# Performance work log

Hardware: AMD Instinct MI355X
Metric: run time of the kernel (lower is better)

## Reference

```python
import jax, jax.numpy as jnp
import numpy as np

HIDDEN = 4096
N_HEADS = 32
N_KV_HEADS = 8
HEAD_DIM = 128
ROPE_THETA = 10000.0


def setup_inputs() -> dict:
    key = jax.random.key(0)
    ks = jax.random.split(key, 5)
    B, S = 1, 2048
    scale = 0.02
    return {
        "hidden_states": jax.random.normal(ks[0], (B, S, HIDDEN), dtype=jnp.float32),
        "q_w": jax.random.normal(ks[1], (N_HEADS * HEAD_DIM, HIDDEN), dtype=jnp.float32) * scale,
        "k_w": jax.random.normal(ks[2], (N_KV_HEADS * HEAD_DIM, HIDDEN), dtype=jnp.float32) * scale,
        "v_w": jax.random.normal(ks[3], (N_KV_HEADS * HEAD_DIM, HIDDEN), dtype=jnp.float32) * scale,
        "o_w": jax.random.normal(ks[4], (HIDDEN, N_HEADS * HEAD_DIM), dtype=jnp.float32) * scale,
        "position_ids": jnp.arange(S, dtype=jnp.int64 if jax.config.jax_enable_x64 else jnp.int32)[None, :],
    }


def _rotate_half(x):
    h = x.shape[-1] // 2
    return jnp.concatenate((-x[..., h:], x[..., :h]), axis=-1)


def _rope_cos_sin(position_ids, dtype):
    # default rope: inv_freq = theta^(-arange(0,hd,2)/hd), attention_scaling = 1
    inv_freq = 1.0 / (ROPE_THETA ** (jnp.arange(0, HEAD_DIM, 2, dtype=jnp.float32) / HEAD_DIM))
    freqs = position_ids.astype(jnp.float32)[:, :, None] * inv_freq[None, None, :]  # [B,S,hd/2]
    emb = jnp.concatenate((freqs, freqs), axis=-1)  # [B,S,hd]
    return jnp.cos(emb).astype(dtype), jnp.sin(emb).astype(dtype)


def reference(hidden_states, q_w, k_w, v_w, o_w, position_ids):
    B, S, _ = hidden_states.shape
    n_rep = N_HEADS // N_KV_HEADS

    q = (hidden_states @ q_w.T).reshape(B, S, N_HEADS, HEAD_DIM).transpose(0, 2, 1, 3)
    k = (hidden_states @ k_w.T).reshape(B, S, N_KV_HEADS, HEAD_DIM).transpose(0, 2, 1, 3)
    v = (hidden_states @ v_w.T).reshape(B, S, N_KV_HEADS, HEAD_DIM).transpose(0, 2, 1, 3)

    cos, sin = _rope_cos_sin(position_ids, hidden_states.dtype)
    cos = cos[:, None, :, :]  # unsqueeze head dim
    sin = sin[:, None, :, :]
    q = q * cos + _rotate_half(q) * sin
    k = k * cos + _rotate_half(k) * sin

    # repeat_kv (GQA)
    k = jnp.repeat(k, n_rep, axis=1)  # [B,H,S,hd]
    v = jnp.repeat(v, n_rep, axis=1)

    scale = HEAD_DIM ** -0.5
    scores = jnp.einsum("bhqd,bhkd->bhqk", q, k) * scale  # [B,H,S,S]
    causal = jnp.tril(jnp.ones((S, S), dtype=bool))
    scores = jnp.where(causal[None, None, :, :], scores, jnp.finfo(scores.dtype).min)
    probs = jax.nn.softmax(scores, axis=-1)
    attn = jnp.einsum("bhqk,bhkd->bhqd", probs, v)  # [B,H,S,hd]

    attn = attn.transpose(0, 2, 1, 3).reshape(B, S, N_HEADS * HEAD_DIM)
    return attn @ o_w.T
```

## Files before the change

kernel.cpp:

```cpp
#include <hip/hip_runtime.h>
#include <hip/hip_bf16.h>

#define NH   32
#define NKV  8
#define HD   128
#define SL   2048
#define HID  4096
#define KVW  1024
#define QKVN 6144

typedef __attribute__((ext_vector_type(8))) short short8;
typedef __attribute__((ext_vector_type(4))) float f32x4;

static __device__ __forceinline__ unsigned short f2bf(float f){
  union { float f; unsigned int i; } v; v.f = f;
  unsigned int r = v.i + 0x7FFFu + ((v.i >> 16) & 1u);
  return (unsigned short)(r >> 16);
}
static __device__ __forceinline__ float bf2f(unsigned short u){
  union { unsigned int i; float f; } v; v.i = ((unsigned int)u) << 16; return v.f;
}
static __device__ __forceinline__ unsigned int pack2(float lo, float hi){
  return (unsigned int)f2bf(lo) | ((unsigned int)f2bf(hi) << 16);
}
static __device__ __forceinline__ unsigned int cvtpk(float lo, float hi){
  unsigned int d;
  asm("v_cvt_pk_bf16_f32 %0, %1, %2" : "=v"(d) : "v"(lo), "v"(hi));
  return d;
}

static __device__ __forceinline__ void gload_lds16(const void* g, void* l){
  __builtin_amdgcn_global_load_lds(
      (const __attribute__((address_space(1))) void*)g,
      (__attribute__((address_space(3))) void*)l,
      16, 0, 0);
}

__global__ void cast_f32_bf16(const float* __restrict__ src, uint4* __restrict__ dst, int n8){
  int stride = gridDim.x * blockDim.x;
  for (int i = blockIdx.x * blockDim.x + threadIdx.x; i < n8; i += stride){
    float4 a = ((const float4*)src)[2*i + 0];
    float4 b = ((const float4*)src)[2*i + 1];
    uint4 o;
    o.x = pack2(a.x, a.y); o.y = pack2(a.z, a.w);
    o.z = pack2(b.x, b.y); o.w = pack2(b.z, b.w);
    dst[i] = o;
  }
}

__global__ void rope_table_kernel(const int* __restrict__ pos, float2* __restrict__ tab){
  int i = blockIdx.x * blockDim.x + threadIdx.x;
  if (i >= SL * 64) return;
  int s = i >> 6, f = i & 63;
  float inv = expf(-((float)(2 * f) / 128.0f) * 9.210340371976184f);
  float ang = (float)pos[s] * inv;
  float sn, cs;
  sincosf(ang, &sn, &cs);
  tab[i] = make_float2(cs, sn);
}

__global__ void rope_apply_kernel(unsigned short* x, const float2* __restrict__ tab,
                                  int nheads, int rowstride){
  int i = blockIdx.x * blockDim.x + threadIdx.x;
  int total = SL * nheads * 8;
  if (i >= total) return;
  int fb = (i & 7) * 8;
  int t = i >> 3;
  int h = t % nheads;
  int s = t / nheads;
  size_t base = (size_t)s * rowstride + h * HD;
  short8 x1 = *(const short8*)&x[base + fb];
  short8 x2 = *(const short8*)&x[base + fb + 64];
  const float2* tb = &tab[s * 64 + fb];
  short8 o1, o2;
#pragma unroll
  for (int j = 0; j < 8; ++j){
    float2 cs = tb[j];
    float a = bf2f((unsigned short)x1[j]);
    float b = bf2f((unsigned short)x2[j]);
    o1[j] = (short)f2bf(a * cs.x - b * cs.y);
    o2[j] = (short)f2bf(b * cs.x + a * cs.y);
  }
  *(short8*)&x[base + fb]      = o1;
  *(short8*)&x[base + fb + 64] = o2;
}

template<int BN, bool F32OUT>
__global__ __launch_bounds__(256) void gemm_bt(
  const unsigned short* __restrict__ A,
  const unsigned short* __restrict__ B,
  void* __restrict__ Cp, int M, int N, int K)
{
  constexpr int NFR = BN / 32;
  __shared__ __align__(16) unsigned short As[2][128 * 32];
  __shared__ __align__(16) unsigned short Bs[2][BN * 32];
  const int tid = threadIdx.x;
  const int lane = tid & 63, wid = tid >> 6;
  const int g = lane >> 4, c15 = lane & 15;
  const int wr = wid >> 1, wc = wid & 1;

  const int gx = gridDim.x, gy = gridDim.y;
  const int nwg = gx * gy;
  const int lin = blockIdx.y * gx + blockIdx.x;
  int mb, nb;
  const int cpx = nwg >> 3;
  const int RN  = cpx >> 3;
  if (RN > 0 && (gy & 7) == 0 && (cpx & 7) == 0 && gx % RN == 0 && (8 % (gx / RN)) == 0){
    int xcd = lin & 7, j = lin >> 3;
    int nrc = gx / RN;
    int rr = xcd / nrc, rc = xcd % nrc;
    mb = rr * 8 + (j & 7);
    nb = rc * RN + (j >> 3);
  } else { mb = lin / gx; nb = lin % gx; }
  const int m0 = mb * 128, n0 = nb * BN;

  const int srowA = wid * 32 + (lane >> 2);
  const int srowB = wid * (BN / 4) + (lane >> 2);
  const int scol  = (lane & 3) * 8;
  const unsigned short* Ag = &A[(size_t)(m0 + srowA) * K + scol];
  const unsigned short* Bg = &B[(size_t)(n0 + srowB) * K + scol];
  const size_t K16 = (size_t)16 * K;

  f32x4 acc[4][NFR] = {};

  gload_lds16(Ag,       &As[0][wid * 1024]);
  gload_lds16(Ag + K16, &As[0][wid * 1024 + 512]);
#pragma unroll
  for (int q = 0; q < BN / 64; ++q)
    gload_lds16(Bg + q * K16, &Bs[0][wid * (BN / 4) * 32 + q * 512]);
  __syncthreads();

  const int nk = K >> 5;
  for (int t = 0; t < nk; ++t){
    const int cur = t & 1;
    if (t + 1 < nk){
      const unsigned short* a2 = Ag + (size_t)(t + 1) * 32;
      const unsigned short* b2 = Bg + (size_t)(t + 1) * 32;
      const int nb2 = cur ^ 1;
      gload_lds16(a2,       &As[nb2][wid * 1024]);
      gload_lds16(a2 + K16, &As[nb2][wid * 1024 + 512]);
#pragma unroll
      for (int q = 0; q < BN / 64; ++q)
        gload_lds16(b2 + q * K16, &Bs[nb2][wid * (BN / 4) * 32 + q * 512]);
    }
    short8 af[4], bfr[NFR];
#pragma unroll
    for (int m = 0; m < 4; ++m)
      af[m] = *(const short8*)(&As[cur][(wr * 64 + m * 16 + c15) * 32 + g * 8]);
#pragma unroll
    for (int n = 0; n < NFR; ++n)
      bfr[n] = *(const short8*)(&Bs[cur][(wc * (BN / 2) + n * 16 + c15) * 32 + g * 8]);
#pragma unroll
    for (int m = 0; m < 4; ++m)
#pragma unroll
      for (int n = 0; n < NFR; ++n)
        acc[m][n] = __builtin_amdgcn_mfma_f32_16x16x32_bf16(af[m], bfr[n], acc[m][n], 0, 0, 0);
    __syncthreads();
  }

#pragma unroll
  for (int m = 0; m < 4; ++m)
#pragma unroll
    for (int n = 0; n < NFR; ++n){
      int row = m0 + wr * 64 + m * 16 + g * 4;
      int col = n0 + wc * (BN / 2) + n * 16 + c15;
      f32x4 v = acc[m][n];
      if (F32OUT){
        float* C = (float*)Cp;
#pragma unroll
        for (int r = 0; r < 4; ++r) C[(size_t)(row + r) * N + col] = v[r];
      } else {
        unsigned short* C = (unsigned short*)Cp;
#pragma unroll
        for (int r = 0; r < 4; ++r) C[(size_t)(row + r) * N + col] = f2bf(v[r]);
      }
    }
}

__global__ void transpose_v_kernel(const unsigned short* __restrict__ v, int vstride,
                                   unsigned short* __restrict__ vt){
  __shared__ unsigned short t[64][65];
  int h  = blockIdx.z;
  int d0 = blockIdx.y * 64;
  int s0 = blockIdx.x * 64;
  int c  = threadIdx.x & 63;
  int r0 = threadIdx.x >> 6;
#pragma unroll
  for (int r = r0; r < 64; r += 4) t[r][c] = v[(size_t)(s0 + r) * vstride + h * HD + d0 + c];
  __syncthreads();
#pragma unroll
  for (int r = r0; r < 64; r += 4) vt[(size_t)(h * HD + d0 + r) * SL + s0 + c] = t[c][r];
}

__global__ __launch_bounds__(512, 4) void flash_attn_kernel(
  const unsigned short* __restrict__ Q,
  const unsigned short* __restrict__ Kb,
  const unsigned short* __restrict__ Vt,
  unsigned short* __restrict__ O)
{
  __shared__ __align__(16) unsigned short Ks[2][64 * 128];
  __shared__ __align__(16) unsigned short Vs[2][128 * 64];
  const int tid = threadIdx.x, lane = tid & 63, wid = tid >> 6;
  const int g = lane >> 4, c15 = lane & 15;
  const int kvh = blockIdx.x;
  const int yy = blockIdx.y;
  const int qb = (yy < 32) ? (63 - yy) : (yy - 32);
  const int h = kvh * 4 + (wid & 3);
  const int rg = wid >> 2;
  const int q0 = qb * 32;
  const int qg = q0 + rg * 16 + c15;

  short8 aq[4];
  {
    size_t qrow = (size_t)qg * QKVN + h * HD;
#pragma unroll
    for (int kk = 0; kk < 4; ++kk)
      aq[kk] = *(const short8*)(&Q[qrow + kk * 32 + g * 8]);
  }

  const int krow = tid >> 3, kcol = (tid & 7) * 8;
  const int vrow = tid >> 2, vcol = (tid & 3) * 8;
  const unsigned short* Kgb = Kb + (size_t)kvh * HD;
  const unsigned short* Vgb = Vt + ((size_t)kvh * HD + vrow) * SL;

  auto loadKV = [&](int kt, uint4& a, uint4& b, uint4& c, uint4& d){
    const unsigned short* kg = Kgb + (size_t)(kt * 64 + krow) * QKVN + kcol;
    a = *(const uint4*)kg; b = *(const uint4*)(kg + 64);
    const unsigned short* vg = Vgb + kt * 64 + vcol;
    c = *(const uint4*)vg; d = *(const uint4*)(vg + 32);
  };
  auto writeKV = [&](int buf, uint4 a, uint4 b, uint4 c, uint4 d){
    *(uint4*)((char*)&Ks[buf][0] + krow * 256 + (( kcol * 2       ) ^ ((krow & 7) << 4))) = a;
    *(uint4*)((char*)&Ks[buf][0] + krow * 256 + (((kcol * 2) + 128) ^ ((krow & 7) << 4))) = b;
    *(uint4*)((char*)&Vs[buf][0] + vrow * 128 + (( vcol * 2       ) ^ ((vrow & 7) << 4))) = c;
    *(uint4*)((char*)&Vs[buf][0] + vrow * 128 + (((vcol * 2) +  64) ^ ((vrow & 7) << 4))) = d;
  };

  float m_i = -1e30f, l_i = 0.f;
  f32x4 oacc[8];
#pragma unroll
  for (int df = 0; df < 8; ++df) oacc[df] = (f32x4){0.f, 0.f, 0.f, 0.f};

  const float scl2 = 0.08838834764831845f * 1.4426950408889634f;
  const int nt = (q0 + 31) / 64 + 1;

  uint4 kr0, kr1, vr0, vr1;
  loadKV(0, kr0, kr1, vr0, vr1);
  writeKV(0, kr0, kr1, vr0, vr1);
  if (nt > 1) loadKV(1, kr0, kr1, vr0, vr1);
  __syncthreads();

  for (int kt = 0; kt < nt; ++kt){
    const int cur = kt & 1, nxt = cur ^ 1;
    if (kt + 1 < nt) writeKV(nxt, kr0, kr1, vr0, vr1);
    if (kt + 2 < nt) loadKV(kt + 2, kr0, kr1, vr0, vr1);

    f32x4 sc[4];
    __builtin_amdgcn_s_setprio(1);
#pragma unroll
    for (int f = 0; f < 4; ++f){
      sc[f] = (f32x4){0.f, 0.f, 0.f, 0.f};
#pragma unroll
      for (int kk = 0; kk < 4; ++kk){
        short8 bk = *(const short8*)((const char*)&Ks[cur][0] + (f * 16 + c15) * 256 +
                                     ((kk * 64 + g * 16) ^ ((c15 & 7) << 4)));
        sc[f] = __builtin_amdgcn_mfma_f32_16x16x32_bf16(bk, aq[kk], sc[f], 0, 0, 0);
      }
    }
    __builtin_amdgcn_s_setprio(0);

    float p[4][4];
    if (kt * 64 + 63 <= q0 + rg * 16){
#pragma unroll
      for (int f = 0; f < 4; ++f)
#pragma unroll
        for (int r = 0; r < 4; ++r) p[f][r] = sc[f][r] * scl2;
    } else {
#pragma unroll
      for (int f = 0; f < 4; ++f)
#pragma unroll
        for (int r = 0; r < 4; ++r){
          int kvg = kt * 64 + f * 16 + g * 4 + r;
          p[f][r] = (kvg <= qg) ? sc[f][r] * scl2 : -1e30f;
        }
    }

    float pmax = p[0][0];
#pragma unroll
    for (int f = 0; f < 4; ++f)
#pragma unroll
      for (int r = 0; r < 4; ++r) pmax = fmaxf(pmax, p[f][r]);
    pmax = fmaxf(pmax, __shfl_xor(pmax, 16, 64));
    pmax = fmaxf(pmax, __shfl_xor(pmax, 32, 64));

    if (!__all(pmax - m_i <= 8.0f)){
      float mnew = fmaxf(m_i, pmax);
      float cf = exp2f(m_i - mnew);
      float cfr[4];
#pragma unroll
      for (int r = 0; r < 4; ++r) cfr[r] = __shfl(cf, (lane & 48) | (g * 4 + r), 64);
#pragma unroll
      for (int df = 0; df < 8; ++df)
#pragma unroll
        for (int r = 0; r < 4; ++r) oacc[df][r] *= cfr[r];
      l_i *= cf;
      m_i = mnew;
    }

    float lsum = 0.f;
#pragma unroll
    for (int f = 0; f < 4; ++f)
#pragma unroll
      for (int r = 0; r < 4; ++r){ float e = exp2f(p[f][r] - m_i); p[f][r] = e; lsum += e; }
    lsum += __shfl_xor(lsum, 16, 64);
    lsum += __shfl_xor(lsum, 32, 64);
    l_i += lsum;

    unsigned int pd[4][2];
#pragma unroll
    for (int f = 0; f < 4; ++f){
      pd[f][0] = cvtpk(p[f][0], p[f][1]);
      pd[f][1] = cvtpk(p[f][2], p[f][3]);
    }

    const int src0 = ((g & 1) << 5) | c15;
    const int src1 = src0 + 16;
    const bool hiF = (g >= 2);
#pragma unroll
    for (int kk = 0; kk < 2; ++kk){
      union { unsigned int u[4]; short8 s8; } pa;
#pragma unroll
      for (int pr = 0; pr < 2; ++pr){
        unsigned int a0 = __shfl((int)pd[2 * kk + 0][pr], src0, 64);
        unsigned int b0 = __shfl((int)pd[2 * kk + 1][pr], src0, 64);
        unsigned int a1 = __shfl((int)pd[2 * kk + 0][pr], src1, 64);
        unsigned int b1 = __shfl((int)pd[2 * kk + 1][pr], src1, 64);
        pa.u[pr]     = hiF ? b0 : a0;
        pa.u[2 + pr] = hiF ? b1 : a1;
      }
      __builtin_amdgcn_s_setprio(1);
#pragma unroll
      for (int df = 0; df < 8; ++df){
        short8 bv = *(const short8*)((const char*)&Vs[cur][0] + (df * 16 + c15) * 128 +
                                     ((kk * 64 + g * 16) ^ ((c15 & 7) << 4)));
        oacc[df] = __builtin_amdgcn_mfma_f32_16x16x32_bf16(pa.s8, bv, oacc[df], 0, 0, 0);
      }
      __builtin_amdgcn_s_setprio(0);
    }
    __syncthreads();
  }

  float lr[4];
#pragma unroll
  for (int r = 0; r < 4; ++r) lr[r] = __shfl(l_i, (lane & 48) | (g * 4 + r), 64);
#pragma unroll
  for (int df = 0; df < 8; ++df)
#pragma unroll
    for (int r = 0; r < 4; ++r){
      int row = q0 + rg * 16 + g * 4 + r;
      O[(size_t)row * HID + h * HD + df * 16 + c15] = f2bf(oacc[df][r] / lr[r]);
    }
}

extern "C" void kernel_launch(void* const* d_in, const int* in_sizes, int n_in,
                              void* d_out, int out_size, void* d_ws, size_t ws_size,
                              hipStream_t stream)
{
  const float* hs  = (const float*)d_in[0];
  const float* qw  = (const float*)d_in[1];
  const float* kw  = (const float*)d_in[2];
  const float* vw  = (const float*)d_in[3];
  const float* ow  = (const float*)d_in[4];
  const int*   pos = (const int*)d_in[5];

  char* w = (char*)d_ws;
  auto alloc = [&](size_t bytes){ char* p = w; w += (bytes + 255) & ~(size_t)255; return p; };
  unsigned short* xb   = (unsigned short*)alloc((size_t)SL * HID * 2);
  unsigned short* wqkv = (unsigned short*)alloc((size_t)QKVN * HID * 2);
  unsigned short* owb  = (unsigned short*)alloc((size_t)HID * HID * 2);
  unsigned short* qkv  = (unsigned short*)alloc((size_t)SL * QKVN * 2);
  unsigned short* vt   = (unsigned short*)alloc((size_t)SL * KVW * 2);
  unsigned short* ab   = (unsigned short*)alloc((size_t)SL * HID * 2);
  float2*         tab  = (float2*)alloc((size_t)SL * 64 * sizeof(float2));

  auto cast = [&](const float* s, unsigned short* d, long n){
    int n8 = (int)(n / 8);
    int blocks = (n8 + 255) / 256; if (blocks > 2048) blocks = 2048;
    cast_f32_bf16<<<blocks, 256, 0, stream>>>(s, (uint4*)d, n8);
  };
  cast(hs, xb, (long)SL * HID);
  cast(qw, wqkv,                              (long)HID * HID);
  cast(kw, wqkv + (size_t)HID * HID,          (long)KVW * HID);
  cast(vw, wqkv + (size_t)(HID + KVW) * HID,  (long)KVW * HID);
  cast(ow, owb,                               (long)HID * HID);

  rope_table_kernel<<<(SL * 64 + 255) / 256, 256, 0, stream>>>(pos, tab);

  gemm_bt<128, false><<<dim3(QKVN / 128, SL / 128), 256, 0, stream>>>(xb, wqkv, qkv, SL, QKVN, HID);

  rope_apply_kernel<<<(SL * 40 * 8 + 255) / 256, 256, 0, stream>>>(qkv, tab, 40, QKVN);

  transpose_v_kernel<<<dim3(SL / 64, HD / 64, NKV), 256, 0, stream>>>(qkv + HID + KVW, QKVN, vt);

  flash_attn_kernel<<<dim3(NKV, SL / 32), 512, 0, stream>>>(qkv, qkv + HID, vt, ab);

  gemm_bt<128, true><<<dim3(HID / 128, SL / 128), 256, 0, stream>>>(ab, owb, d_out, SL, HID, HID);
}
```

Before: 343.9 us.

## Have each flash-attention wave process two query row-groups to reuse K/V fragments

The attention block shrinks from 8 waves to 4. Each wave now handles both 16-row query halves for one head, so every K and V fragment read from LDS feeds two MFMAs instead of one. This halves LDS read traffic per MFMA. The cost is double the accumulator and score registers per wave and fewer waves per block, which may lower occupancy and latency hiding, and each thread now issues more global loads per K/V tile.

```diff
diff --git a/kernel.cpp b/kernel.cpp
--- a/kernel.cpp
+++ b/kernel.cpp
@@ -192,7 +192,7 @@
   for (int r = r0; r < 64; r += 4) vt[(size_t)(h * HD + d0 + r) * SL + s0 + c] = t[c][r];
 }
 
-__global__ __launch_bounds__(512, 4) void flash_attn_kernel(
+__global__ __launch_bounds__(256, 2) void flash_attn_kernel(
   const unsigned short* __restrict__ Q,
   const unsigned short* __restrict__ Kb,
   const unsigned short* __restrict__ Vt,
@@ -205,122 +205,138 @@
   const int kvh = blockIdx.x;
   const int yy = blockIdx.y;
   const int qb = (yy < 32) ? (63 - yy) : (yy - 32);
-  const int h = kvh * 4 + (wid & 3);
-  const int rg = wid >> 2;
+  const int h = kvh * 4 + wid;
   const int q0 = qb * 32;
-  const int qg = q0 + rg * 16 + c15;
-
-  short8 aq[4];
-  {
-    size_t qrow = (size_t)qg * QKVN + h * HD;
+
+  short8 aq[2][4];
+#pragma unroll
+  for (int qh = 0; qh < 2; ++qh){
+    size_t qrow = (size_t)(q0 + qh * 16 + c15) * QKVN + h * HD;
 #pragma unroll
     for (int kk = 0; kk < 4; ++kk)
-      aq[kk] = *(const short8*)(&Q[qrow + kk * 32 + g * 8]);
-  }
-
-  const int krow = tid >> 3, kcol = (tid & 7) * 8;
-  const int vrow = tid >> 2, vcol = (tid & 3) * 8;
+      aq[qh][kk] = *(const short8*)(&Q[qrow + kk * 32 + g * 8]);
+  }
+
+  const int krow = tid >> 2;
+  const int vrow = tid >> 1;
   const unsigned short* Kgb = Kb + (size_t)kvh * HD;
   const unsigned short* Vgb = Vt + ((size_t)kvh * HD + vrow) * SL;
 
-  auto loadKV = [&](int kt, uint4& a, uint4& b, uint4& c, uint4& d){
-    const unsigned short* kg = Kgb + (size_t)(kt * 64 + krow) * QKVN + kcol;
-    a = *(const uint4*)kg; b = *(const uint4*)(kg + 64);
-    const unsigned short* vg = Vgb + kt * 64 + vcol;
-    c = *(const uint4*)vg; d = *(const uint4*)(vg + 32);
+  uint4 kr[4], vr[4];
+  auto loadKV = [&](int kt){
+    const unsigned short* kg = Kgb + (size_t)(kt * 64 + krow) * QKVN;
+    const unsigned short* vg = Vgb + kt * 64;
+#pragma unroll
+    for (int j = 0; j < 4; ++j){
+      kr[j] = *(const uint4*)(kg + ((tid & 3) * 4 + j) * 8);
+      vr[j] = *(const uint4*)(vg + ((tid & 1) * 4 + j) * 8);
+    }
   };
-  auto writeKV = [&](int buf, uint4 a, uint4 b, uint4 c, uint4 d){
-    *(uint4*)((char*)&Ks[buf][0] + krow * 256 + (( kcol * 2       ) ^ ((krow & 7) << 4))) = a;
-    *(uint4*)((char*)&Ks[buf][0] + krow * 256 + (((kcol * 2) + 128) ^ ((krow & 7) << 4))) = b;
-    *(uint4*)((char*)&Vs[buf][0] + vrow * 128 + (( vcol * 2       ) ^ ((vrow & 7) << 4))) = c;
-    *(uint4*)((char*)&Vs[buf][0] + vrow * 128 + (((vcol * 2) +  64) ^ ((vrow & 7) << 4))) = d;
+  auto writeKV = [&](int buf){
+#pragma unroll
+    for (int j = 0; j < 4; ++j){
+      int ks = (tid & 3) * 4 + j;
+      int vs = (tid & 1) * 4 + j;
+      *(uint4*)((char*)&Ks[buf][0] + krow * 256 + ((ks * 16) ^ ((krow & 7) << 4))) = kr[j];
+      *(uint4*)((char*)&Vs[buf][0] + vrow * 128 + ((vs * 16) ^ ((vrow & 7) << 4))) = vr[j];
+    }
   };
 
-  float m_i = -1e30f, l_i = 0.f;
-  f32x4 oacc[8];
-#pragma unroll
-  for (int df = 0; df < 8; ++df) oacc[df] = (f32x4){0.f, 0.f, 0.f, 0.f};
+  float m_i[2] = {-1e30f, -1e30f}, l_i[2] = {0.f, 0.f};
+  f32x4 oacc[2][8];
+#pragma unroll
+  for (int qh = 0; qh < 2; ++qh)
+#pragma unroll
+    for (int df = 0; df < 8; ++df) oacc[qh][df] = (f32x4){0.f, 0.f, 0.f, 0.f};
 
   const float scl2 = 0.08838834764831845f * 1.4426950408889634f;
   const int nt = (q0 + 31) / 64 + 1;
 
-  uint4 kr0, kr1, vr0, vr1;
-  loadKV(0, kr0, kr1, vr0, vr1);
-  writeKV(0, kr0, kr1, vr0, vr1);
-  if (nt > 1) loadKV(1, kr0, kr1, vr0, vr1);
+  loadKV(0);
+  writeKV(0);
+  if (nt > 1) loadKV(1);
   __syncthreads();
 
   for (int kt = 0; kt < nt; ++kt){
     const int cur = kt & 1, nxt = cur ^ 1;
-    if (kt + 1 < nt) writeKV(nxt, kr0, kr1, vr0, vr1);
-    if (kt + 2 < nt) loadKV(kt + 2, kr0, kr1, vr0, vr1);
-
-    f32x4 sc[4];
+    if (kt + 1 < nt) writeKV(nxt);
+    if (kt + 2 < nt) loadKV(kt + 2);
+
+    f32x4 sc[2][4];
+#pragma unroll
+    for (int qh = 0; qh < 2; ++qh)
+#pragma unroll
+      for (int f = 0; f < 4; ++f) sc[qh][f] = (f32x4){0.f, 0.f, 0.f, 0.f};
     __builtin_amdgcn_s_setprio(1);
 #pragma unroll
-    for (int f = 0; f < 4; ++f){
-      sc[f] = (f32x4){0.f, 0.f, 0.f, 0.f};
+    for (int f = 0; f < 4; ++f)
 #pragma unroll
       for (int kk = 0; kk < 4; ++kk){
         short8 bk = *(const short8*)((const char*)&Ks[cur][0] + (f * 16 + c15) * 256 +
                                      ((kk * 64 + g * 16) ^ ((c15 & 7) << 4)));
-        sc[f] = __builtin_amdgcn_mfma_f32_16x16x32_bf16(bk, aq[kk], sc[f], 0, 0, 0);
-      }
-    }
+        sc[0][f] = __builtin_amdgcn_mfma_f32_16x16x32_bf16(bk, aq[0][kk], sc[0][f], 0, 0, 0);
+        sc[1][f] = __builtin_amdgcn_mfma_f32_16x16x32_bf16(bk, aq[1][kk], sc[1][f], 0, 0, 0);
+      }
     __builtin_amdgcn_s_setprio(0);
 
-    float p[4][4];
-    if (kt * 64 + 63 <= q0 + rg * 16){
+    float p[2][4][4];
+    unsigned int pd[2][4][2];
+#pragma unroll
+    for (int qh = 0; qh < 2; ++qh){
+      const int qg = q0 + qh * 16 + c15;
+      if (kt * 64 + 63 <= q0 + qh * 16){
+#pragma unroll
+        for (int f = 0; f < 4; ++f)
+#pragma unroll
+          for (int r = 0; r < 4; ++r) p[qh][f][r] = sc[qh][f][r] * scl2;
+      } else {
+#pragma unroll
+        for (int f = 0; f < 4; ++f)
+#pragma unroll
+          for (int r = 0; r < 4; ++r){
+            int kvg = kt * 64 + f * 16 + g * 4 + r;
+            p[qh][f][r] = (kvg <= qg) ? sc[qh][f][r] * scl2 : -1e30f;
+          }
+      }
+
+      float pmax = p[qh][0][0];
 #pragma unroll
       for (int f = 0; f < 4; ++f)
 #pragma unroll
-        for (int r = 0; r < 4; ++r) p[f][r] = sc[f][r] * scl2;
-    } else {
+        for (int r = 0; r < 4; ++r) pmax = fmaxf(pmax, p[qh][f][r]);
+      pmax = fmaxf(pmax, __shfl_xor(pmax, 16, 64));
+      pmax = fmaxf(pmax, __shfl_xor(pmax, 32, 64));
+
+      if (!__all(pmax - m_i[qh] <= 8.0f)){
+        float mnew = fmaxf(m_i[qh], pmax);
+        float cf = exp2f(m_i[qh] - mnew);
+        float cfr[4];
+#pragma unroll
+        for (int r = 0; r < 4; ++r) cfr[r] = __shfl(cf, (lane & 48) | (g * 4 + r), 64);
+#pragma unroll
+        for (int df = 0; df < 8; ++df)
+#pragma unroll
+          for (int r = 0; r < 4; ++r) oacc[qh][df][r] *= cfr[r];
+        l_i[qh] *= cf;
+        m_i[qh] = mnew;
+      }
+
+      float lsum = 0.f;
 #pragma unroll
       for (int f = 0; f < 4; ++f)
 #pragma unroll
         for (int r = 0; r < 4; ++r){
-          int kvg = kt * 64 + f * 16 + g * 4 + r;
-          p[f][r] = (kvg <= qg) ? sc[f][r] * scl2 : -1e30f;
+          float e = exp2f(p[qh][f][r] - m_i[qh]); p[qh][f][r] = e; lsum += e;
         }
-    }
-
-    float pmax = p[0][0];
-#pragma unroll
-    for (int f = 0; f < 4; ++f)
-#pragma unroll
-      for (int r = 0; r < 4; ++r) pmax = fmaxf(pmax, p[f][r]);
-    pmax = fmaxf(pmax, __shfl_xor(pmax, 16, 64));
-    pmax = fmaxf(pmax, __shfl_xor(pmax, 32, 64));
-
-    if (!__all(pmax - m_i <= 8.0f)){
-      float mnew = fmaxf(m_i, pmax);
-      float cf = exp2f(m_i - mnew);
-      float cfr[4];
-#pragma unroll
-      for (int r = 0; r < 4; ++r) cfr[r] = __shfl(cf, (lane & 48) | (g * 4 + r), 64);
-#pragma unroll
-      for (int df = 0; df < 8; ++df)
-#pragma unroll
-        for (int r = 0; r < 4; ++r) oacc[df][r] *= cfr[r];
-      l_i *= cf;
-      m_i = mnew;
-    }
-
-    float lsum = 0.f;
-#pragma unroll
-    for (int f = 0; f < 4; ++f)
-#pragma unroll
-      for (int r = 0; r < 4; ++r){ float e = exp2f(p[f][r] - m_i); p[f][r] = e; lsum += e; }
-    lsum += __shfl_xor(lsum, 16, 64);
-    lsum += __shfl_xor(lsum, 32, 64);
-    l_i += lsum;
-
-    unsigned int pd[4][2];
-#pragma unroll
-    for (int f = 0; f < 4; ++f){
-      pd[f][0] = cvtpk(p[f][0], p[f][1]);
-      pd[f][1] = cvtpk(p[f][2], p[f][3]);
+      lsum += __shfl_xor(lsum, 16, 64);
+      lsum += __shfl_xor(lsum, 32, 64);
+      l_i[qh] += lsum;
+
+#pragma unroll
+      for (int f = 0; f < 4; ++f){
+        pd[qh][f][0] = cvtpk(p[qh][f][0], p[qh][f][1]);
+        pd[qh][f][1] = cvtpk(p[qh][f][2], p[qh][f][3]);
+      }
     }
 
     const int src0 = ((g & 1) << 5) | c15;
@@ -328,38 +344,44 @@
     const bool hiF = (g >= 2);
 #pragma unroll
     for (int kk = 0; kk < 2; ++kk){
-      union { unsigned int u[4]; short8 s8; } pa;
-#pragma unroll
-      for (int pr = 0; pr < 2; ++pr){
-        unsigned int a0 = __shfl((int)pd[2 * kk + 0][pr], src0, 64);
-        unsigned int b0 = __shfl((int)pd[2 * kk + 1][pr], src0, 64);
-        unsigned int a1 = __shfl((int)pd[2 * kk + 0][pr], src1, 64);
-        unsigned int b1 = __shfl((int)pd[2 * kk + 1][pr], src1, 64);
-        pa.u[pr]     = hiF ? b0 : a0;
-        pa.u[2 + pr] = hiF ? b1 : a1;
-      }
+      union { unsigned int u[4]; short8 s8; } pa[2];
+#pragma unroll
+      for (int qh = 0; qh < 2; ++qh)
+#pragma unroll
+        for (int pr = 0; pr < 2; ++pr){
+          unsigned int a0 = __shfl((int)pd[qh][2 * kk + 0][pr], src0, 64);
+          unsigned int b0 = __shfl((int)pd[qh][2 * kk + 1][pr], src0, 64);
+          unsigned int a1 = __shfl((int)pd[qh][2 * kk + 0][pr], src1, 64);
+          unsigned int b1 = __shfl((int)pd[qh][2 * kk + 1][pr], src1, 64);
+          pa[qh].u[pr]     = hiF ? b0 : a0;
+          pa[qh].u[2 + pr] = hiF ? b1 : a1;
+        }
       __builtin_amdgcn_s_setprio(1);
 #pragma unroll
       for (int df = 0; df < 8; ++df){
         short8 bv = *(const short8*)((const char*)&Vs[cur][0] + (df * 16 + c15) * 128 +
                                      ((kk * 64 + g * 16) ^ ((c15 & 7) << 4)));
-        oacc[df] = __builtin_amdgcn_mfma_f32_16x16x32_bf16(pa.s8, bv, oacc[df], 0, 0, 0);
+        oacc[0][df] = __builtin_amdgcn_mfma_f32_16x16x32_bf16(pa[0].s8, bv, oacc[0][df], 0, 0, 0);
+        oacc[1][df] = __builtin_amdgcn_mfma_f32_16x16x32_bf16(pa[1].s8, bv, oacc[1][df], 0, 0, 0);
       }
       __builtin_amdgcn_s_setprio(0);
     }
     __syncthreads();
   }
 
-  float lr[4];
-#pragma unroll
-  for (int r = 0; r < 4; ++r) lr[r] = __shfl(l_i, (lane & 48) | (g * 4 + r), 64);
-#pragma unroll
-  for (int df = 0; df < 8; ++df)
-#pragma unroll
-    for (int r = 0; r < 4; ++r){
-      int row = q0 + rg * 16 + g * 4 + r;
-      O[(size_t)row * HID + h * HD + df * 16 + c15] = f2bf(oacc[df][r] / lr[r]);
-    }
+#pragma unroll
+  for (int qh = 0; qh < 2; ++qh){
+    float lr[4];
+#pragma unroll
+    for (int r = 0; r < 4; ++r) lr[r] = __shfl(l_i[qh], (lane & 48) | (g * 4 + r), 64);
+#pragma unroll
+    for (int df = 0; df < 8; ++df)
+#pragma unroll
+      for (int r = 0; r < 4; ++r){
+        int row = q0 + qh * 16 + g * 4 + r;
+        O[(size_t)row * HID + h * HD + df * 16 + c15] = f2bf(oacc[qh][df][r] / lr[r]);
+      }
+  }
 }
 
 extern "C" void kernel_launch(void* const* d_in, const int* in_sizes, int n_in,
@@ -402,7 +424,7 @@
 
   transpose_v_kernel<<<dim3(SL / 64, HD / 64, NKV), 256, 0, stream>>>(qkv + HID + KVW, QKVN, vt);
 
-  flash_attn_kernel<<<dim3(NKV, SL / 32), 512, 0, stream>>>(qkv, qkv + HID, vt, ab);
+  flash_attn_kernel<<<dim3(NKV, SL / 32), 256, 0, stream>>>(qkv, qkv + HID, vt, ab);
 
   gemm_bt<128, true><<<dim3(HID / 128, SL / 128), 256, 0, stream>>>(ab, owb, d_out, SL, HID, HID);
 }
```

Result: slower. 396.4 us (+15.3%).

## Use direct global-to-LDS loads with 128-wide KV tiles and skip masked fragments

Applied to the files above, without the earlier changes.

Flash attention now stages K and V tiles of 128 keys (instead of 64) into a single LDS buffer, using direct global-to-LDS loads (gload_lds16) with an XOR slot swizzle. The register-staged double buffering is removed. MFMA fragments that lie entirely above the causal diagonal are skipped in both the QK and PV products. This cuts per-tile loop and register-staging overhead and avoids wasted MFMA work on masked blocks. In exchange, tile loads are no longer overlapped with compute: each iteration waits behind two barriers. The larger LDS footprint (64KB) may also limit occupancy.

```diff
diff --git a/kernel.cpp b/kernel.cpp
--- a/kernel.cpp
+++ b/kernel.cpp
@@ -198,8 +198,8 @@
   const unsigned short* __restrict__ Vt,
   unsigned short* __restrict__ O)
 {
-  __shared__ __align__(16) unsigned short Ks[2][64 * 128];
-  __shared__ __align__(16) unsigned short Vs[2][128 * 64];
+  __shared__ __align__(16) unsigned short Ks[128 * 128];
+  __shared__ __align__(16) unsigned short Vs[128 * 128];
   const int tid = threadIdx.x, lane = tid & 63, wid = tid >> 6;
   const int g = lane >> 4, c15 = lane & 15;
   const int kvh = blockIdx.x;
@@ -209,6 +209,7 @@
   const int rg = wid >> 2;
   const int q0 = qb * 32;
   const int qg = q0 + rg * 16 + c15;
+  const int qmax = q0 + rg * 16 + 15;
 
   short8 aq[4];
   {
@@ -218,23 +219,10 @@
       aq[kk] = *(const short8*)(&Q[qrow + kk * 32 + g * 8]);
   }
 
-  const int krow = tid >> 3, kcol = (tid & 7) * 8;
-  const int vrow = tid >> 2, vcol = (tid & 3) * 8;
-  const unsigned short* Kgb = Kb + (size_t)kvh * HD;
-  const unsigned short* Vgb = Vt + ((size_t)kvh * HD + vrow) * SL;
-
-  auto loadKV = [&](int kt, uint4& a, uint4& b, uint4& c, uint4& d){
-    const unsigned short* kg = Kgb + (size_t)(kt * 64 + krow) * QKVN + kcol;
-    a = *(const uint4*)kg; b = *(const uint4*)(kg + 64);
-    const unsigned short* vg = Vgb + kt * 64 + vcol;
-    c = *(const uint4*)vg; d = *(const uint4*)(vg + 32);
-  };
-  auto writeKV = [&](int buf, uint4 a, uint4 b, uint4 c, uint4 d){
-    *(uint4*)((char*)&Ks[buf][0] + krow * 256 + (( kcol * 2       ) ^ ((krow & 7) << 4))) = a;
-    *(uint4*)((char*)&Ks[buf][0] + krow * 256 + (((kcol * 2) + 128) ^ ((krow & 7) << 4))) = b;
-    *(uint4*)((char*)&Vs[buf][0] + vrow * 128 + (( vcol * 2       ) ^ ((vrow & 7) << 4))) = c;
-    *(uint4*)((char*)&Vs[buf][0] + vrow * 128 + (((vcol * 2) +  64) ^ ((vrow & 7) << 4))) = d;
-  };
+  const int srow4 = lane >> 4;
+  const int slotE = (lane & 15) ^ srow4;
+  const unsigned short* Kg0 = Kb + (size_t)kvh * HD;
+  const unsigned short* Vg0 = Vt + (size_t)kvh * HD * SL;
 
   float m_i = -1e30f, l_i = 0.f;
   f32x4 oacc[8];
@@ -242,52 +230,54 @@
   for (int df = 0; df < 8; ++df) oacc[df] = (f32x4){0.f, 0.f, 0.f, 0.f};
 
   const float scl2 = 0.08838834764831845f * 1.4426950408889634f;
-  const int nt = (q0 + 31) / 64 + 1;
-
-  uint4 kr0, kr1, vr0, vr1;
-  loadKV(0, kr0, kr1, vr0, vr1);
-  writeKV(0, kr0, kr1, vr0, vr1);
-  if (nt > 1) loadKV(1, kr0, kr1, vr0, vr1);
-  __syncthreads();
-
+  const int nt = (q0 + 31) / 128 + 1;
   for (int kt = 0; kt < nt; ++kt){
-    const int cur = kt & 1, nxt = cur ^ 1;
-    if (kt + 1 < nt) writeKV(nxt, kr0, kr1, vr0, vr1);
-    if (kt + 2 < nt) loadKV(kt + 2, kr0, kr1, vr0, vr1);
-
-    f32x4 sc[4];
+    __syncthreads();
+#pragma unroll
+    for (int j = 0; j < 4; ++j){
+      const int rbase = wid * 16 + j * 4;
+      const int col = (slotE ^ ((j & 1) << 2)) * 8;
+      const int row = rbase + srow4;
+      gload_lds16(Kg0 + (size_t)(kt * 128 + row) * QKVN + col, &Ks[rbase * 128]);
+      gload_lds16(Vg0 + (size_t)row * SL + kt * 128 + col,     &Vs[rbase * 128]);
+    }
+    __syncthreads();
+
+    f32x4 sc[8];
     __builtin_amdgcn_s_setprio(1);
 #pragma unroll
-    for (int f = 0; f < 4; ++f){
+    for (int f = 0; f < 8; ++f){
       sc[f] = (f32x4){0.f, 0.f, 0.f, 0.f};
-#pragma unroll
-      for (int kk = 0; kk < 4; ++kk){
-        short8 bk = *(const short8*)((const char*)&Ks[cur][0] + (f * 16 + c15) * 256 +
-                                     ((kk * 64 + g * 16) ^ ((c15 & 7) << 4)));
-        sc[f] = __builtin_amdgcn_mfma_f32_16x16x32_bf16(bk, aq[kk], sc[f], 0, 0, 0);
+      if (kt * 128 + f * 16 <= qmax){
+#pragma unroll
+        for (int kk = 0; kk < 4; ++kk){
+          short8 bk = *(const short8*)((const char*)Ks + (f * 16 + c15) * 256 +
+                                       ((kk * 64 + g * 16) ^ ((c15 & 7) << 4)));
+          sc[f] = __builtin_amdgcn_mfma_f32_16x16x32_bf16(bk, aq[kk], sc[f], 0, 0, 0);
+        }
       }
     }
     __builtin_amdgcn_s_setprio(0);
 
-    float p[4][4];
-    if (kt * 64 + 63 <= q0 + rg * 16){
-#pragma unroll
-      for (int f = 0; f < 4; ++f)
+    float p[8][4];
+    if (kt * 128 + 127 <= q0 + rg * 16){
+#pragma unroll
+      for (int f = 0; f < 8; ++f)
 #pragma unroll
         for (int r = 0; r < 4; ++r) p[f][r] = sc[f][r] * scl2;
     } else {
 #pragma unroll
-      for (int f = 0; f < 4; ++f)
+      for (int f = 0; f < 8; ++f)
 #pragma unroll
         for (int r = 0; r < 4; ++r){
-          int kvg = kt * 64 + f * 16 + g * 4 + r;
+          int kvg = kt * 128 + f * 16 + g * 4 + r;
           p[f][r] = (kvg <= qg) ? sc[f][r] * scl2 : -1e30f;
         }
     }
 
     float pmax = p[0][0];
 #pragma unroll
-    for (int f = 0; f < 4; ++f)
+    for (int f = 0; f < 8; ++f)
 #pragma unroll
       for (int r = 0; r < 4; ++r) pmax = fmaxf(pmax, p[f][r]);
     pmax = fmaxf(pmax, __shfl_xor(pmax, 16, 64));
@@ -309,16 +299,16 @@
 
     float lsum = 0.f;
 #pragma unroll
-    for (int f = 0; f < 4; ++f)
+    for (int f = 0; f < 8; ++f)
 #pragma unroll
       for (int r = 0; r < 4; ++r){ float e = exp2f(p[f][r] - m_i); p[f][r] = e; lsum += e; }
     lsum += __shfl_xor(lsum, 16, 64);
     lsum += __shfl_xor(lsum, 32, 64);
     l_i += lsum;
 
-    unsigned int pd[4][2];
-#pragma unroll
-    for (int f = 0; f < 4; ++f){
+    unsigned int pd[8][2];
+#pragma unroll
+    for (int f = 0; f < 8; ++f){
       pd[f][0] = cvtpk(p[f][0], p[f][1]);
       pd[f][1] = cvtpk(p[f][2], p[f][3]);
     }
@@ -327,27 +317,28 @@
     const int src1 = src0 + 16;
     const bool hiF = (g >= 2);
 #pragma unroll
-    for (int kk = 0; kk < 2; ++kk){
-      union { unsigned int u[4]; short8 s8; } pa;
-#pragma unroll
-      for (int pr = 0; pr < 2; ++pr){
-        unsigned int a0 = __shfl((int)pd[2 * kk + 0][pr], src0, 64);
-        unsigned int b0 = __shfl((int)pd[2 * kk + 1][pr], src0, 64);
-        unsigned int a1 = __shfl((int)pd[2 * kk + 0][pr], src1, 64);
-        unsigned int b1 = __shfl((int)pd[2 * kk + 1][pr], src1, 64);
-        pa.u[pr]     = hiF ? b0 : a0;
-        pa.u[2 + pr] = hiF ? b1 : a1;
+    for (int kk = 0; kk < 4; ++kk){
+      if (kt * 128 + kk * 32 <= qmax){
+        union { unsigned int u[4]; short8 s8; } pa;
+#pragma unroll
+        for (int pr = 0; pr < 2; ++pr){
+          unsigned int a0 = __shfl((int)pd[2 * kk + 0][pr], src0, 64);
+          unsigned int b0 = __shfl((int)pd[2 * kk + 1][pr], src0, 64);
+          unsigned int a1 = __shfl((int)pd[2 * kk + 0][pr], src1, 64);
+          unsigned int b1 = __shfl((int)pd[2 * kk + 1][pr], src1, 64);
+          pa.u[pr]     = hiF ? b0 : a0;
+          pa.u[2 + pr] = hiF ? b1 : a1;
+        }
+        __builtin_amdgcn_s_setprio(1);
+#pragma unroll
+        for (int df = 0; df < 8; ++df){
+          short8 bv = *(const short8*)((const char*)Vs + (df * 16 + c15) * 256 +
+                                       ((kk * 64 + g * 16) ^ ((c15 & 7) << 4)));
+          oacc[df] = __builtin_amdgcn_mfma_f32_16x16x32_bf16(pa.s8, bv, oacc[df], 0, 0, 0);
+        }
+        __builtin_amdgcn_s_setprio(0);
       }
-      __builtin_amdgcn_s_setprio(1);
-#pragma unroll
-      for (int df = 0; df < 8; ++df){
-        short8 bv = *(const short8*)((const char*)&Vs[cur][0] + (df * 16 + c15) * 128 +
-                                     ((kk * 64 + g * 16) ^ ((c15 & 7) << 4)));
-        oacc[df] = __builtin_amdgcn_mfma_f32_16x16x32_bf16(pa.s8, bv, oacc[df], 0, 0, 0);
-      }
-      __builtin_amdgcn_s_setprio(0);
-    }
-    __syncthreads();
+    }
   }
 
   float lr[4];
```

After: 389.3 us. +13.2%, slower.

## Skip fully masked causal MFMA fragments and fuse five cast launches into one

Applied to the files above, without the earlier changes.

In the attention kernel, the QK^T and PV MFMA blocks are now skipped when a 16-column key fragment or 32-key chunk lies entirely above the causal diagonal for the wave's query rows. This removes wasted matrix work on the diagonal tile. Separately, the five fp32-to-bf16 cast launches are merged into one segmented kernel, which cuts launch overhead and tail effects. In exchange, the flash loop gains branches that may interfere with instruction scheduling.

```diff
diff --git a/kernel.cpp b/kernel.cpp
--- a/kernel.cpp
+++ b/kernel.cpp
@@ -36,15 +36,25 @@
       16, 0, 0);
 }
 
-__global__ void cast_f32_bf16(const float* __restrict__ src, uint4* __restrict__ dst, int n8){
+struct CastSegs {
+  const float* src[5];
+  unsigned short* dst[5];
+  int off[6];
+};
+__global__ void cast_all(CastSegs cs, int total8){
   int stride = gridDim.x * blockDim.x;
-  for (int i = blockIdx.x * blockDim.x + threadIdx.x; i < n8; i += stride){
-    float4 a = ((const float4*)src)[2*i + 0];
-    float4 b = ((const float4*)src)[2*i + 1];
+  for (int i = blockIdx.x * blockDim.x + threadIdx.x; i < total8; i += stride){
+    int s = 0;
+#pragma unroll
+    for (int t = 1; t < 5; ++t) s += (i >= cs.off[t]) ? 1 : 0;
+    int j = i - cs.off[s];
+    const float4* sp = (const float4*)cs.src[s];
+    float4 a = sp[2*j + 0];
+    float4 b = sp[2*j + 1];
     uint4 o;
     o.x = pack2(a.x, a.y); o.y = pack2(a.z, a.w);
     o.z = pack2(b.x, b.y); o.w = pack2(b.z, b.w);
-    dst[i] = o;
+    ((uint4*)cs.dst[s])[j] = o;
   }
 }
 
@@ -209,6 +219,7 @@
   const int rg = wid >> 2;
   const int q0 = qb * 32;
   const int qg = q0 + rg * 16 + c15;
+  const int qmax = q0 + rg * 16 + 15;
 
   short8 aq[4];
   {
@@ -260,11 +271,13 @@
 #pragma unroll
     for (int f = 0; f < 4; ++f){
       sc[f] = (f32x4){0.f, 0.f, 0.f, 0.f};
-#pragma unroll
-      for (int kk = 0; kk < 4; ++kk){
-        short8 bk = *(const short8*)((const char*)&Ks[cur][0] + (f * 16 + c15) * 256 +
-                                     ((kk * 64 + g * 16) ^ ((c15 & 7) << 4)));
-        sc[f] = __builtin_amdgcn_mfma_f32_16x16x32_bf16(bk, aq[kk], sc[f], 0, 0, 0);
+      if (kt * 64 + f * 16 <= qmax){
+#pragma unroll
+        for (int kk = 0; kk < 4; ++kk){
+          short8 bk = *(const short8*)((const char*)&Ks[cur][0] + (f * 16 + c15) * 256 +
+                                       ((kk * 64 + g * 16) ^ ((c15 & 7) << 4)));
+          sc[f] = __builtin_amdgcn_mfma_f32_16x16x32_bf16(bk, aq[kk], sc[f], 0, 0, 0);
+        }
       }
     }
     __builtin_amdgcn_s_setprio(0);
@@ -328,24 +341,26 @@
     const bool hiF = (g >= 2);
 #pragma unroll
     for (int kk = 0; kk < 2; ++kk){
-      union { unsigned int u[4]; short8 s8; } pa;
-#pragma unroll
-      for (int pr = 0; pr < 2; ++pr){
-        unsigned int a0 = __shfl((int)pd[2 * kk + 0][pr], src0, 64);
-        unsigned int b0 = __shfl((int)pd[2 * kk + 1][pr], src0, 64);
-        unsigned int a1 = __shfl((int)pd[2 * kk + 0][pr], src1, 64);
-        unsigned int b1 = __shfl((int)pd[2 * kk + 1][pr], src1, 64);
-        pa.u[pr]     = hiF ? b0 : a0;
-        pa.u[2 + pr] = hiF ? b1 : a1;
+      if (kt * 64 + kk * 32 <= qmax){
+        union { unsigned int u[4]; short8 s8; } pa;
+#pragma unroll
+        for (int pr = 0; pr < 2; ++pr){
+          unsigned int a0 = __shfl((int)pd[2 * kk + 0][pr], src0, 64);
+          unsigned int b0 = __shfl((int)pd[2 * kk + 1][pr], src0, 64);
+          unsigned int a1 = __shfl((int)pd[2 * kk + 0][pr], src1, 64);
+          unsigned int b1 = __shfl((int)pd[2 * kk + 1][pr], src1, 64);
+          pa.u[pr]     = hiF ? b0 : a0;
+          pa.u[2 + pr] = hiF ? b1 : a1;
+        }
+        __builtin_amdgcn_s_setprio(1);
+#pragma unroll
+        for (int df = 0; df < 8; ++df){
+          short8 bv = *(const short8*)((const char*)&Vs[cur][0] + (df * 16 + c15) * 128 +
+                                       ((kk * 64 + g * 16) ^ ((c15 & 7) << 4)));
+          oacc[df] = __builtin_amdgcn_mfma_f32_16x16x32_bf16(pa.s8, bv, oacc[df], 0, 0, 0);
+        }
+        __builtin_amdgcn_s_setprio(0);
       }
-      __builtin_amdgcn_s_setprio(1);
-#pragma unroll
-      for (int df = 0; df < 8; ++df){
-        short8 bv = *(const short8*)((const char*)&Vs[cur][0] + (df * 16 + c15) * 128 +
-                                     ((kk * 64 + g * 16) ^ ((c15 & 7) << 4)));
-        oacc[df] = __builtin_amdgcn_mfma_f32_16x16x32_bf16(pa.s8, bv, oacc[df], 0, 0, 0);
-      }
-      __builtin_amdgcn_s_setprio(0);
     }
     __syncthreads();
   }
@@ -383,16 +398,17 @@
   unsigned short* ab   = (unsigned short*)alloc((size_t)SL * HID * 2);
   float2*         tab  = (float2*)alloc((size_t)SL * 64 * sizeof(float2));
 
-  auto cast = [&](const float* s, unsigned short* d, long n){
-    int n8 = (int)(n / 8);
-    int blocks = (n8 + 255) / 256; if (blocks > 2048) blocks = 2048;
-    cast_f32_bf16<<<blocks, 256, 0, stream>>>(s, (uint4*)d, n8);
-  };
-  cast(hs, xb, (long)SL * HID);
-  cast(qw, wqkv,                              (long)HID * HID);
-  cast(kw, wqkv + (size_t)HID * HID,          (long)KVW * HID);
-  cast(vw, wqkv + (size_t)(HID + KVW) * HID,  (long)KVW * HID);
-  cast(ow, owb,                               (long)HID * HID);
+  CastSegs cs;
+  cs.src[0] = hs;  cs.dst[0] = xb;
+  cs.src[1] = qw;  cs.dst[1] = wqkv;
+  cs.src[2] = kw;  cs.dst[2] = wqkv + (size_t)HID * HID;
+  cs.src[3] = vw;  cs.dst[3] = wqkv + (size_t)(HID + KVW) * HID;
+  cs.src[4] = ow;  cs.dst[4] = owb;
+  int n8s[5] = { SL * HID / 8, HID * HID / 8, KVW * HID / 8, KVW * HID / 8, HID * HID / 8 };
+  cs.off[0] = 0;
+  for (int i = 0; i < 5; ++i) cs.off[i + 1] = cs.off[i] + n8s[i];
+  int total8 = cs.off[5];
+  cast_all<<<2048, 256, 0, stream>>>(cs, total8);
 
   rope_table_kernel<<<(SL * 64 + 255) / 256, 256, 0, stream>>>(pos, tab);
 
```

Measured after the change: 337.4 us (median of 2 runs). Within noise of the previous version (-1.9%).
